# Kernel tuning notes

Measured on AMD Instinct MI355X. Metric: run time of the kernel, lower is better.

Reference implementation:

```python
import jax, jax.numpy as jnp
import numpy as np

N_NODES = 50000
IN_CH = 512
OUT_CH = 512
N_EDGES = 800000


def setup_inputs() -> dict:
    key = jax.random.key(0)
    ks = jax.random.split(key, 6)
    x = jax.random.normal(ks[0], (N_NODES, IN_CH), dtype=jnp.float32)
    edge_index = jax.random.randint(ks[1], (2, N_EDGES), 0, N_NODES, dtype=jnp.int64)
    edge_index_2 = jax.random.randint(ks[2], (2, N_EDGES), 0, N_NODES, dtype=jnp.int64)
    W1 = jax.random.normal(ks[3], (IN_CH, OUT_CH), dtype=jnp.float32) * (1.0 / np.sqrt(IN_CH))
    b1 = jnp.zeros((OUT_CH,), dtype=jnp.float32)
    W2 = jax.random.normal(ks[4], (IN_CH, OUT_CH), dtype=jnp.float32) * (1.0 / np.sqrt(IN_CH))
    b2 = jnp.zeros((OUT_CH,), dtype=jnp.float32)
    return {"x": x, "edge_index": edge_index, "edge_index_2": edge_index_2,
            "W1": W1, "b1": b1, "W2": W2, "b2": b2}


def _sgconv(x, edge_index, W, b, K=2):
    # PyG SGConv: K rounds of D^-1/2 (A+I) D^-1/2 propagation, then Linear.
    N = x.shape[0]
    loops = jnp.arange(N, dtype=edge_index.dtype)
    row = jnp.concatenate([edge_index[0], loops])  # source nodes
    col = jnp.concatenate([edge_index[1], loops])  # destination nodes
    deg = jax.ops.segment_sum(jnp.ones_like(col, dtype=x.dtype), col, num_segments=N)
    deg_inv_sqrt = jnp.where(deg > 0, jnp.where(deg > 0, deg, 1.0) ** -0.5, 0.0)
    norm = deg_inv_sqrt[row] * deg_inv_sqrt[col]  # [E+N]
    h = x
    for _ in range(K):
        h = jax.ops.segment_sum(h[row] * norm[:, None], col, num_segments=N)
    return h @ W + b


def reference(x, edge_index, edge_index_2, W1, b1, W2, b2):
    x1 = _sgconv(x, edge_index, W1, b1)
    x2 = _sgconv(x, edge_index_2, W2, b2)
    logits = jax.nn.softmax(x1, axis=1)
    logits_2 = jax.nn.softmax(x2, axis=1)
    predictions = jnp.argmax(logits, axis=1)
    return (logits, logits_2, predictions)
```

## Files before the change

### kernel.cpp

```cpp
#include <hip/hip_runtime.h>
#include <hip/hip_bf16.h>
#include <cstdint>
#include <cstddef>

#define N_NODES 50000
#define N_EDGES 800000
#define CH 512

typedef __attribute__((ext_vector_type(8))) short bf16x8;
typedef __attribute__((ext_vector_type(4))) float f32x4;

__device__ inline unsigned short f2b(float f) {
    __hip_bfloat16 h = __float2bfloat16(f);
    return *(unsigned short*)&h;
}
__device__ inline float blo(unsigned int u) {
    union { unsigned int i; float f; } v; v.i = u << 16; return v.f;
}
__device__ inline float bhi(unsigned int u) {
    union { unsigned int i; float f; } v; v.i = u & 0xffff0000u; return v.f;
}
__device__ inline unsigned int pack2(unsigned short a, unsigned short b) {
    return (unsigned)a | ((unsigned)b << 16);
}


__global__ __launch_bounds__(256) void count_col(const int* __restrict__ col, int* __restrict__ cnt) {
    int e = blockIdx.x * 256 + threadIdx.x;
    if (e < N_EDGES) atomicAdd(&cnt[col[e]], 1);
}

__global__ __launch_bounds__(256) void make_dinv(const int* __restrict__ cnt, float* __restrict__ dinv) {
    int i = blockIdx.x * 256 + threadIdx.x;
    if (i < N_NODES) dinv[i] = rsqrtf((float)(cnt[i] + 1));
}

__global__ __launch_bounds__(1024) void scan_offsets(const int* __restrict__ cnt, int* __restrict__ offs) {
    __shared__ int wsum[16];
    __shared__ int s_carry;
    int tid = threadIdx.x;
    int lane = tid & 63, wid = tid >> 6;
    if (tid == 0) s_carry = 0;
    __syncthreads();
    const int n = N_NODES;
    for (int c0 = 0; c0 < n; c0 += 1024) {
        int i = c0 + tid;
        int v = (i < n) ? cnt[i] : 0;
        int incl = v;
        #pragma unroll
        for (int d = 1; d < 64; d <<= 1) {
            int t = __shfl_up(incl, d, 64);
            if (lane >= d) incl += t;
        }
        if (lane == 63) wsum[wid] = incl;
        __syncthreads();
        int wbase = 0;
        for (int w = 0; w < wid; ++w) wbase += wsum[w];
        int excl = s_carry + wbase + incl - v;
        if (i < n) offs[i] = excl;
        int ctot = wbase + incl;
        __syncthreads();
        if (tid == 1023) s_carry += ctot;
        __syncthreads();
    }
    if (tid == 0) offs[n] = s_carry;
}

__global__ __launch_bounds__(256) void fill_csr(const int* __restrict__ edges,
                                                const int* __restrict__ offs,
                                                int* __restrict__ cursor,
                                                const float* __restrict__ dinv,
                                                int* __restrict__ srcs,
                                                float* __restrict__ enorm) {
    int e = blockIdx.x * 256 + threadIdx.x;
    if (e >= N_EDGES) return;
    int r = edges[e];
    int c = edges[N_EDGES + e];
    int p = offs[c] + atomicAdd(&cursor[c], 1);
    srcs[p] = r;
    enorm[p] = dinv[r] * dinv[c];
}


__global__ __launch_bounds__(256) void convert_x_bf16(const float* __restrict__ x, unsigned short* __restrict__ xb) {
    int i8 = blockIdx.x * 256 + threadIdx.x;
    const float4* x4 = (const float4*)x;
    float4 a = x4[2 * i8], b = x4[2 * i8 + 1];
    unsigned int o[4];
    o[0] = pack2(f2b(a.x), f2b(a.y));
    o[1] = pack2(f2b(a.z), f2b(a.w));
    o[2] = pack2(f2b(b.x), f2b(b.y));
    o[3] = pack2(f2b(b.z), f2b(b.w));
    ((uint4*)xb)[i8] = make_uint4(o[0], o[1], o[2], o[3]);
}

__global__ __launch_bounds__(256) void convert_w_t(const float* __restrict__ W, unsigned short* __restrict__ Wt) {
    int id = blockIdx.x * 256 + threadIdx.x;
    int k = id >> 9, n = id & 511;
    Wt[(size_t)n * 512 + k] = f2b(W[(size_t)k * 512 + n]);
}

__global__ __launch_bounds__(256) void convert_w_t_split(const float* __restrict__ W,
                                                         unsigned short* __restrict__ Wth,
                                                         unsigned short* __restrict__ Wtl) {
    int id = blockIdx.x * 256 + threadIdx.x;
    int k = id >> 9, n = id & 511;
    float f = W[(size_t)k * 512 + n];
    unsigned short hb = f2b(f);
    union { unsigned int u; float ff; } t; t.u = (unsigned)hb << 16;
    float lo = f - t.ff;
    Wth[(size_t)n * 512 + k] = hb;
    Wtl[(size_t)n * 512 + k] = f2b(lo);
}


__global__ __launch_bounds__(128) void propagate(const float* __restrict__ h, float* __restrict__ out,
                                                 const int* __restrict__ offs,
                                                 const int* __restrict__ srcs,
                                                 const float* __restrict__ enorm,
                                                 const float* __restrict__ dinv) {
    int node = blockIdx.x;
    int t = threadIdx.x;
    const float4* h4 = (const float4*)h;
    float di = dinv[node];
    float w0 = di * di;
    float4 v = h4[(size_t)node * 128 + t];
    float4 acc = make_float4(v.x * w0, v.y * w0, v.z * w0, v.w * w0);
    int e0 = offs[node], e1 = offs[node + 1];
    int e = e0;
    int eu = e0 + ((e1 - e0) & ~3);
    for (; e < eu; e += 4) {
        int s0 = srcs[e], s1 = srcs[e + 1], s2 = srcs[e + 2], s3 = srcs[e + 3];
        float wa = enorm[e], wb = enorm[e + 1], wc = enorm[e + 2], wd = enorm[e + 3];
        float4 u0 = h4[(size_t)s0 * 128 + t];
        float4 u1 = h4[(size_t)s1 * 128 + t];
        float4 u2 = h4[(size_t)s2 * 128 + t];
        float4 u3 = h4[(size_t)s3 * 128 + t];
        acc.x += u0.x * wa; acc.y += u0.y * wa; acc.z += u0.z * wa; acc.w += u0.w * wa;
        acc.x += u1.x * wb; acc.y += u1.y * wb; acc.z += u1.z * wb; acc.w += u1.w * wb;
        acc.x += u2.x * wc; acc.y += u2.y * wc; acc.z += u2.z * wc; acc.w += u2.w * wc;
        acc.x += u3.x * wd; acc.y += u3.y * wd; acc.z += u3.z * wd; acc.w += u3.w * wd;
    }
    for (; e < e1; ++e) {
        int s = srcs[e];
        float w = enorm[e];
        float4 u = h4[(size_t)s * 128 + t];
        acc.x += u.x * w; acc.y += u.y * w; acc.z += u.z * w; acc.w += u.w * w;
    }
    ((float4*)out)[(size_t)node * 128 + t] = acc;
}


__global__ __launch_bounds__(128) void propagate_bf16(const unsigned short* __restrict__ hb,
                                                      unsigned short* __restrict__ outb,
                                                      const int* __restrict__ offs,
                                                      const int* __restrict__ srcs,
                                                      const float* __restrict__ enorm,
                                                      const float* __restrict__ dinv) {
    int node = blockIdx.x * 2 + (threadIdx.x >> 6);
    int lane = threadIdx.x & 63;
    const uint4* h16 = (const uint4*)hb;
    float di = dinv[node];
    float w0 = di * di;
    float acc[8];
    uint4 sv = h16[(size_t)node * 64 + lane];
    acc[0] = blo(sv.x) * w0; acc[1] = bhi(sv.x) * w0;
    acc[2] = blo(sv.y) * w0; acc[3] = bhi(sv.y) * w0;
    acc[4] = blo(sv.z) * w0; acc[5] = bhi(sv.z) * w0;
    acc[6] = blo(sv.w) * w0; acc[7] = bhi(sv.w) * w0;
    int e0 = offs[node], e1 = offs[node + 1];
    int e = e0;
    int eu = e0 + ((e1 - e0) & ~3);
    for (; e < eu; e += 4) {
        int s0 = srcs[e], s1 = srcs[e + 1], s2 = srcs[e + 2], s3 = srcs[e + 3];
        float wa = enorm[e], wb = enorm[e + 1], wc = enorm[e + 2], wd = enorm[e + 3];
        uint4 u0 = h16[(size_t)s0 * 64 + lane];
        uint4 u1 = h16[(size_t)s1 * 64 + lane];
        uint4 u2 = h16[(size_t)s2 * 64 + lane];
        uint4 u3 = h16[(size_t)s3 * 64 + lane];
        acc[0] += blo(u0.x) * wa; acc[1] += bhi(u0.x) * wa;
        acc[2] += blo(u0.y) * wa; acc[3] += bhi(u0.y) * wa;
        acc[4] += blo(u0.z) * wa; acc[5] += bhi(u0.z) * wa;
        acc[6] += blo(u0.w) * wa; acc[7] += bhi(u0.w) * wa;
        acc[0] += blo(u1.x) * wb; acc[1] += bhi(u1.x) * wb;
        acc[2] += blo(u1.y) * wb; acc[3] += bhi(u1.y) * wb;
        acc[4] += blo(u1.z) * wb; acc[5] += bhi(u1.z) * wb;
        acc[6] += blo(u1.w) * wb; acc[7] += bhi(u1.w) * wb;
        acc[0] += blo(u2.x) * wc; acc[1] += bhi(u2.x) * wc;
        acc[2] += blo(u2.y) * wc; acc[3] += bhi(u2.y) * wc;
        acc[4] += blo(u2.z) * wc; acc[5] += bhi(u2.z) * wc;
        acc[6] += blo(u2.w) * wc; acc[7] += bhi(u2.w) * wc;
        acc[0] += blo(u3.x) * wd; acc[1] += bhi(u3.x) * wd;
        acc[2] += blo(u3.y) * wd; acc[3] += bhi(u3.y) * wd;
        acc[4] += blo(u3.z) * wd; acc[5] += bhi(u3.z) * wd;
        acc[6] += blo(u3.w) * wd; acc[7] += bhi(u3.w) * wd;
    }
    for (; e < e1; ++e) {
        int s = srcs[e];
        float w = enorm[e];
        uint4 u = h16[(size_t)s * 64 + lane];
        acc[0] += blo(u.x) * w; acc[1] += bhi(u.x) * w;
        acc[2] += blo(u.y) * w; acc[3] += bhi(u.y) * w;
        acc[4] += blo(u.z) * w; acc[5] += bhi(u.z) * w;
        acc[6] += blo(u.w) * w; acc[7] += bhi(u.w) * w;
    }
    unsigned int o0 = pack2(f2b(acc[0]), f2b(acc[1]));
    unsigned int o1 = pack2(f2b(acc[2]), f2b(acc[3]));
    unsigned int o2 = pack2(f2b(acc[4]), f2b(acc[5]));
    unsigned int o3 = pack2(f2b(acc[6]), f2b(acc[7]));
    ((uint4*)outb)[(size_t)node * 64 + lane] = make_uint4(o0, o1, o2, o3);
}


#define BM2 128
#define BN2 64
#define BK2 32
#define LDP 40

__global__ __launch_bounds__(256) void gemm_bf16(const unsigned short* __restrict__ Ab,
                                                 const unsigned short* __restrict__ Wt,
                                                 const float* __restrict__ bias,
                                                 float* __restrict__ C) {
    __shared__ short Alds[BM2 * LDP];
    __shared__ short Blds[BN2 * LDP];
    int tid = threadIdx.x;
    int lane = tid & 63;
    int wid = tid >> 6;
    int wm = wid & 1;
    int wn = wid >> 1;
    int bm = blockIdx.x * BM2;
    int bn = blockIdx.y * BN2;

    f32x4 acc[4][2] = {};

    int arow0 = tid >> 2, aq = tid & 3;
    int brow = tid >> 2, bq = tid & 3;

    for (int k0 = 0; k0 < CH; k0 += BK2) {
        #pragma unroll
        for (int h = 0; h < 2; ++h) {
            int row = arow0 + h * 64;
            int gr = bm + row;
            uint4 v = make_uint4(0u, 0u, 0u, 0u);
            if (gr < N_NODES) v = *(const uint4*)&Ab[(size_t)gr * CH + k0 + aq * 8];
            *(uint4*)&Alds[row * LDP + aq * 8] = v;
        }
        {
            uint4 v = *(const uint4*)&Wt[(size_t)(bn + brow) * CH + k0 + bq * 8];
            *(uint4*)&Blds[brow * LDP + bq * 8] = v;
        }
        __syncthreads();

        bf16x8 af[4], bf[2];
        #pragma unroll
        for (int mt = 0; mt < 4; ++mt)
            af[mt] = *(const bf16x8*)&Alds[(wm * 64 + mt * 16 + (lane & 15)) * LDP + (lane >> 4) * 8];
        #pragma unroll
        for (int nt = 0; nt < 2; ++nt)
            bf[nt] = *(const bf16x8*)&Blds[(wn * 32 + nt * 16 + (lane & 15)) * LDP + (lane >> 4) * 8];
        #pragma unroll
        for (int mt = 0; mt < 4; ++mt)
            #pragma unroll
            for (int nt = 0; nt < 2; ++nt)
                acc[mt][nt] = __builtin_amdgcn_mfma_f32_16x16x32_bf16(af[mt], bf[nt], acc[mt][nt], 0, 0, 0);
        __syncthreads();
    }

    #pragma unroll
    for (int mt = 0; mt < 4; ++mt) {
        #pragma unroll
        for (int nt = 0; nt < 2; ++nt) {
            int col = bn + wn * 32 + nt * 16 + (lane & 15);
            float bv = bias[col];
            #pragma unroll
            for (int r = 0; r < 4; ++r) {
                int row = bm + wm * 64 + mt * 16 + (lane >> 4) * 4 + r;
                if (row < N_NODES) C[(size_t)row * CH + col] = acc[mt][nt][r] + bv;
            }
        }
    }
}


#define BM3 128
#define BN3 64
#define BK3 32
#define LDP3 40

__global__ __launch_bounds__(256) void gemm_bf16x3(const float* __restrict__ A,
                                                   const unsigned short* __restrict__ Wth,
                                                   const unsigned short* __restrict__ Wtl,
                                                   const float* __restrict__ bias,
                                                   float* __restrict__ C) {
    __shared__ short Ah[BM3 * LDP3];
    __shared__ short Al[BM3 * LDP3];
    __shared__ short Bh[BN3 * LDP3];
    __shared__ short Bl[BN3 * LDP3];
    int tid = threadIdx.x;
    int lane = tid & 63;
    int wid = tid >> 6;
    int wm = wid & 1;
    int wn = wid >> 1;
    int bm = blockIdx.x * BM3;
    int bn = blockIdx.y * BN3;

    f32x4 acc[4][2] = {};

    int arow = tid >> 1, aseg = tid & 1;
    int ga = bm + arow;
    bool aval = ga < N_NODES;
    const float4* A4 = (const float4*)A;
    int brow = tid >> 2, bq = tid & 3;

    for (int k0 = 0; k0 < CH; k0 += BK3) {
        {
            size_t base = (size_t)ga * 128 + (k0 >> 2) + aseg * 4;
            unsigned short h[16], l[16];
            #pragma unroll
            for (int v = 0; v < 4; ++v) {
                float4 f = aval ? A4[base + v] : make_float4(0.f, 0.f, 0.f, 0.f);
                float fs[4] = {f.x, f.y, f.z, f.w};
                #pragma unroll
                for (int j = 0; j < 4; ++j) {
                    unsigned short hb = f2b(fs[j]);
                    union { unsigned int u; float ff; } t; t.u = (unsigned)hb << 16;
                    float lo = fs[j] - t.ff;
                    h[v * 4 + j] = hb;
                    l[v * 4 + j] = f2b(lo);
                }
            }
            uint4 H0 = make_uint4(pack2(h[0], h[1]), pack2(h[2], h[3]), pack2(h[4], h[5]), pack2(h[6], h[7]));
            uint4 H1 = make_uint4(pack2(h[8], h[9]), pack2(h[10], h[11]), pack2(h[12], h[13]), pack2(h[14], h[15]));
            uint4 L0 = make_uint4(pack2(l[0], l[1]), pack2(l[2], l[3]), pack2(l[4], l[5]), pack2(l[6], l[7]));
            uint4 L1 = make_uint4(pack2(l[8], l[9]), pack2(l[10], l[11]), pack2(l[12], l[13]), pack2(l[14], l[15]));
            *(uint4*)&Ah[arow * LDP3 + aseg * 16] = H0;
            *(uint4*)&Ah[arow * LDP3 + aseg * 16 + 8] = H1;
            *(uint4*)&Al[arow * LDP3 + aseg * 16] = L0;
            *(uint4*)&Al[arow * LDP3 + aseg * 16 + 8] = L1;
        }
        *(uint4*)&Bh[brow * LDP3 + bq * 8] = *(const uint4*)&Wth[(size_t)(bn + brow) * CH + k0 + bq * 8];
        *(uint4*)&Bl[brow * LDP3 + bq * 8] = *(const uint4*)&Wtl[(size_t)(bn + brow) * CH + k0 + bq * 8];
        __syncthreads();

        bf16x8 afh[4], afl[4], bfh[2], bfl[2];
        #pragma unroll
        for (int mt = 0; mt < 4; ++mt) {
            int off = (wm * 64 + mt * 16 + (lane & 15)) * LDP3 + (lane >> 4) * 8;
            afh[mt] = *(const bf16x8*)&Ah[off];
            afl[mt] = *(const bf16x8*)&Al[off];
        }
        #pragma unroll
        for (int nt = 0; nt < 2; ++nt) {
            int off = (wn * 32 + nt * 16 + (lane & 15)) * LDP3 + (lane >> 4) * 8;
            bfh[nt] = *(const bf16x8*)&Bh[off];
            bfl[nt] = *(const bf16x8*)&Bl[off];
        }
        #pragma unroll
        for (int mt = 0; mt < 4; ++mt)
            #pragma unroll
            for (int nt = 0; nt < 2; ++nt) {
                acc[mt][nt] = __builtin_amdgcn_mfma_f32_16x16x32_bf16(afh[mt], bfh[nt], acc[mt][nt], 0, 0, 0);
                acc[mt][nt] = __builtin_amdgcn_mfma_f32_16x16x32_bf16(afl[mt], bfh[nt], acc[mt][nt], 0, 0, 0);
                acc[mt][nt] = __builtin_amdgcn_mfma_f32_16x16x32_bf16(afh[mt], bfl[nt], acc[mt][nt], 0, 0, 0);
            }
        __syncthreads();
    }

    #pragma unroll
    for (int mt = 0; mt < 4; ++mt) {
        #pragma unroll
        for (int nt = 0; nt < 2; ++nt) {
            int col = bn + wn * 32 + nt * 16 + (lane & 15);
            float bv = bias[col];
            #pragma unroll
            for (int r = 0; r < 4; ++r) {
                int row = bm + wm * 64 + mt * 16 + (lane >> 4) * 4 + r;
                if (row < N_NODES) C[(size_t)row * CH + col] = acc[mt][nt][r] + bv;
            }
        }
    }
}


#define GAP_THR 2.0e-4f
#define SUSP_CAP 49999

__global__ __launch_bounds__(256) void softmax_rows(const float* __restrict__ X, float* __restrict__ P,
                                                    float* __restrict__ preds,
                                                    int* __restrict__ susp_cnt,
                                                    int* __restrict__ susp_rows) {
    int row = blockIdx.x * 4 + (threadIdx.x >> 6);
    int lane = threadIdx.x & 63;
    if (row >= N_NODES) return;
    const float4* x4 = (const float4*)(X + (size_t)row * CH);
    float4 v0 = x4[lane];
    float4 v1 = x4[lane + 64];
    float vals[8] = {v0.x, v0.y, v0.z, v0.w, v1.x, v1.y, v1.z, v1.w};
    float m = vals[0];
    float m2 = -INFINITY;
    int mi = lane * 4;
    #pragma unroll
    for (int j = 1; j < 8; ++j) {
        int c = (j < 4) ? (lane * 4 + j) : (256 + lane * 4 + (j - 4));
        if (vals[j] > m) { m2 = m; m = vals[j]; mi = c; }
        else if (vals[j] > m2) { m2 = vals[j]; }
    }
    #pragma unroll
    for (int d = 32; d > 0; d >>= 1) {
        float om = __shfl_xor(m, d, 64);
        int oi = __shfl_xor(mi, d, 64);
        float om2 = __shfl_xor(m2, d, 64);
        if (om > m || (om == m && oi < mi)) {
            m2 = fmaxf(m, om2);
            m = om; mi = oi;
        } else {
            m2 = fmaxf(m2, om);
        }
    }
    float s = 0.f;
    float ex[8];
    #pragma unroll
    for (int j = 0; j < 8; ++j) { ex[j] = __expf(vals[j] - m); s += ex[j]; }
    #pragma unroll
    for (int d = 32; d > 0; d >>= 1) s += __shfl_xor(s, d, 64);
    float inv = 1.0f / s;
    float4 o0 = make_float4(ex[0] * inv, ex[1] * inv, ex[2] * inv, ex[3] * inv);
    float4 o1 = make_float4(ex[4] * inv, ex[5] * inv, ex[6] * inv, ex[7] * inv);
    float4* p4 = (float4*)(P + (size_t)row * CH);
    p4[lane] = o0;
    p4[lane + 64] = o1;
    if (preds != nullptr && lane == 0) {
        preds[row] = (float)mi;
        if (m - m2 < GAP_THR) {
            int p = atomicAdd(susp_cnt, 1);
            if (p < SUSP_CAP) susp_rows[p] = row;
        }
    }
}


__global__ __launch_bounds__(256) void fix_preds(const float* __restrict__ A, const float* __restrict__ W,
                                                 const float* __restrict__ bias,
                                                 const int* __restrict__ susp_cnt,
                                                 const int* __restrict__ susp_rows,
                                                 float* __restrict__ preds) {
    __shared__ float rowbuf[8][512];
    __shared__ float rbest[8][4];
    __shared__ int ridx[8][4];
    int cnt = *susp_cnt;
    if (cnt > SUSP_CAP) cnt = SUSP_CAP;
    int tid = threadIdx.x, lane = tid & 63, wid = tid >> 6;
    for (int base = blockIdx.x * 8; base < cnt; base += gridDim.x * 8) {
        int nr = min(8, cnt - base);
        __syncthreads();
        for (int r = 0; r < nr; ++r) {
            int row = susp_rows[base + r];
            if (tid < 128) ((float4*)rowbuf[r])[tid] = ((const float4*)&A[(size_t)row * 512])[tid];
        }
        __syncthreads();
        float best[8]; int bidx[8];
        #pragma unroll
        for (int r = 0; r < 8; ++r) { best[r] = -INFINITY; bidx[r] = 0; }
        for (int cc = 0; cc < 2; ++cc) {
            int c = cc * 256 + tid;
            float bv = bias[c];
            float s[8];
            #pragma unroll
            for (int r = 0; r < 8; ++r) s[r] = bv;
            #pragma unroll 8
            for (int k = 0; k < 512; ++k) {
                float w = W[(size_t)k * 512 + c];
                #pragma unroll
                for (int r = 0; r < 8; ++r) s[r] += rowbuf[r][k] * w;
            }
            #pragma unroll
            for (int r = 0; r < 8; ++r)
                if (s[r] > best[r]) { best[r] = s[r]; bidx[r] = c; }
        }
        #pragma unroll
        for (int r = 0; r < 8; ++r) {
            float b = best[r]; int i = bidx[r];
            #pragma unroll
            for (int d = 32; d > 0; d >>= 1) {
                float ob = __shfl_xor(b, d, 64);
                int oi = __shfl_xor(i, d, 64);
                if (ob > b || (ob == b && oi < i)) { b = ob; i = oi; }
            }
            if (lane == 0) { rbest[r][wid] = b; ridx[r][wid] = i; }
        }
        __syncthreads();
        if (tid < nr) {
            int r = tid;
            float b = rbest[r][0]; int i = ridx[r][0];
            #pragma unroll
            for (int w = 1; w < 4; ++w) {
                if (rbest[r][w] > b || (rbest[r][w] == b && ridx[r][w] < i)) { b = rbest[r][w]; i = ridx[r][w]; }
            }
            preds[susp_rows[base + r]] = (float)i;
        }
    }
}


extern "C" void kernel_launch(void* const* d_in, const int* in_sizes, int n_in,
                              void* d_out, int out_size, void* d_ws, size_t ws_size,
                              hipStream_t stream) {
    const float* x  = (const float*)d_in[0];
    const int*   e1 = (const int*)d_in[1];
    const int*   e2 = (const int*)d_in[2];
    const float* W1 = (const float*)d_in[3];
    const float* b1 = (const float*)d_in[4];
    const float* W2 = (const float*)d_in[5];
    const float* b2 = (const float*)d_in[6];

    float* out     = (float*)d_out;
    float* logits1 = out;
    float* logits2 = out + (size_t)N_NODES * CH;
    float* preds   = out + 2 * (size_t)N_NODES * CH;

    const size_t NEED = 109600016;
    if (ws_size < NEED) return;

    char* ws = (char*)d_ws;
    float* A      = (float*)(ws);
    int*   cnt    = (int*)(ws + 102400000);
    int*   offs   = (int*)(ws + 102600000);
    int*   cursor = (int*)(ws + 102800016);
    float* dinv   = (float*)(ws + 103000016);
    int*   srcs   = (int*)(ws + 103200016);
    float* enorm  = (float*)(ws + 106400016);

    unsigned short* xb  = (unsigned short*)logits1;
    unsigned short* Wtb = (unsigned short*)((char*)logits1 + 51200000);
    unsigned short* h1b = (unsigned short*)A;
    unsigned short* h2b = (unsigned short*)((char*)A + 51200000);

    unsigned short* Wt1h = (unsigned short*)srcs;
    unsigned short* Wt1l = (unsigned short*)enorm;
    int* susp_cnt  = (int*)cursor;
    int* susp_rows = (int*)cursor + 1;

    {
        hipMemsetAsync(cnt, 0, N_NODES * sizeof(int), stream);
        hipMemsetAsync(cursor, 0, N_NODES * sizeof(int), stream);
        count_col<<<(N_EDGES + 255) / 256, 256, 0, stream>>>(e2 + N_EDGES, cnt);
        make_dinv<<<(N_NODES + 255) / 256, 256, 0, stream>>>(cnt, dinv);
        scan_offsets<<<1, 1024, 0, stream>>>(cnt, offs);
        fill_csr<<<(N_EDGES + 255) / 256, 256, 0, stream>>>(e2, offs, cursor, dinv, srcs, enorm);

        convert_x_bf16<<<(N_NODES * CH / 8 + 255) / 256, 256, 0, stream>>>(x, xb);
        convert_w_t<<<(512 * 512) / 256, 256, 0, stream>>>(W2, Wtb);

        propagate_bf16<<<N_NODES / 2, 128, 0, stream>>>(xb, h1b, offs, srcs, enorm, dinv);
        propagate_bf16<<<N_NODES / 2, 128, 0, stream>>>(h1b, h2b, offs, srcs, enorm, dinv);

        dim3 g((N_NODES + BM2 - 1) / BM2, CH / BN2);
        gemm_bf16<<<g, 256, 0, stream>>>(h2b, Wtb, b2, logits2);
        softmax_rows<<<N_NODES / 4, 256, 0, stream>>>(logits2, logits2, nullptr, nullptr, nullptr);
    }

    {
        hipMemsetAsync(cnt, 0, N_NODES * sizeof(int), stream);
        hipMemsetAsync(cursor, 0, N_NODES * sizeof(int), stream);
        count_col<<<(N_EDGES + 255) / 256, 256, 0, stream>>>(e1 + N_EDGES, cnt);
        make_dinv<<<(N_NODES + 255) / 256, 256, 0, stream>>>(cnt, dinv);
        scan_offsets<<<1, 1024, 0, stream>>>(cnt, offs);
        fill_csr<<<(N_EDGES + 255) / 256, 256, 0, stream>>>(e1, offs, cursor, dinv, srcs, enorm);

        propagate<<<N_NODES, 128, 0, stream>>>(x, logits1, offs, srcs, enorm, dinv);
        propagate<<<N_NODES, 128, 0, stream>>>(logits1, A, offs, srcs, enorm, dinv);

        convert_w_t_split<<<(512 * 512) / 256, 256, 0, stream>>>(W1, Wt1h, Wt1l);
        hipMemsetAsync(susp_cnt, 0, sizeof(int), stream);

        dim3 g((N_NODES + BM3 - 1) / BM3, CH / BN3);
        gemm_bf16x3<<<g, 256, 0, stream>>>(A, Wt1h, Wt1l, b1, logits1);
        softmax_rows<<<N_NODES / 4, 256, 0, stream>>>(logits1, logits1, preds, susp_cnt, susp_rows);
        fix_preds<<<400, 256, 0, stream>>>(A, W1, b1, susp_cnt, susp_rows, preds);
    }
}
```

Before: 1.749 ms.

## Widen GEMM tiles to 256 columns, unroll gathers by 8, fold dinv into scan

```diff
diff --git a/kernel.cpp b/kernel.cpp
--- a/kernel.cpp
+++ b/kernel.cpp
@@ -30,12 +30,8 @@
     if (e < N_EDGES) atomicAdd(&cnt[col[e]], 1);
 }
 
-__global__ __launch_bounds__(256) void make_dinv(const int* __restrict__ cnt, float* __restrict__ dinv) {
-    int i = blockIdx.x * 256 + threadIdx.x;
-    if (i < N_NODES) dinv[i] = rsqrtf((float)(cnt[i] + 1));
-}
-
-__global__ __launch_bounds__(1024) void scan_offsets(const int* __restrict__ cnt, int* __restrict__ offs) {
+__global__ __launch_bounds__(1024) void scan_offsets(const int* __restrict__ cnt, int* __restrict__ offs,
+                                                     float* __restrict__ dinv) {
     __shared__ int wsum[16];
     __shared__ int s_carry;
     int tid = threadIdx.x;
@@ -46,6 +42,7 @@
     for (int c0 = 0; c0 < n; c0 += 1024) {
         int i = c0 + tid;
         int v = (i < n) ? cnt[i] : 0;
+        if (i < n) dinv[i] = rsqrtf((float)(v + 1));
         int incl = v;
         #pragma unroll
         for (int d = 1; d < 64; d <<= 1) {
@@ -128,18 +125,19 @@
     float4 acc = make_float4(v.x * w0, v.y * w0, v.z * w0, v.w * w0);
     int e0 = offs[node], e1 = offs[node + 1];
     int e = e0;
-    int eu = e0 + ((e1 - e0) & ~3);
-    for (; e < eu; e += 4) {
-        int s0 = srcs[e], s1 = srcs[e + 1], s2 = srcs[e + 2], s3 = srcs[e + 3];
-        float wa = enorm[e], wb = enorm[e + 1], wc = enorm[e + 2], wd = enorm[e + 3];
-        float4 u0 = h4[(size_t)s0 * 128 + t];
-        float4 u1 = h4[(size_t)s1 * 128 + t];
-        float4 u2 = h4[(size_t)s2 * 128 + t];
-        float4 u3 = h4[(size_t)s3 * 128 + t];
-        acc.x += u0.x * wa; acc.y += u0.y * wa; acc.z += u0.z * wa; acc.w += u0.w * wa;
-        acc.x += u1.x * wb; acc.y += u1.y * wb; acc.z += u1.z * wb; acc.w += u1.w * wb;
-        acc.x += u2.x * wc; acc.y += u2.y * wc; acc.z += u2.z * wc; acc.w += u2.w * wc;
-        acc.x += u3.x * wd; acc.y += u3.y * wd; acc.z += u3.z * wd; acc.w += u3.w * wd;
+    int eu = e0 + ((e1 - e0) & ~7);
+    for (; e < eu; e += 8) {
+        int s[8]; float w[8];
+        #pragma unroll
+        for (int q = 0; q < 8; ++q) { s[q] = srcs[e + q]; w[q] = enorm[e + q]; }
+        float4 u[8];
+        #pragma unroll
+        for (int q = 0; q < 8; ++q) u[q] = h4[(size_t)s[q] * 128 + t];
+        #pragma unroll
+        for (int q = 0; q < 8; ++q) {
+            acc.x += u[q].x * w[q]; acc.y += u[q].y * w[q];
+            acc.z += u[q].z * w[q]; acc.w += u[q].w * w[q];
+        }
     }
     for (; e < e1; ++e) {
         int s = srcs[e];
@@ -170,30 +168,21 @@
     acc[6] = blo(sv.w) * w0; acc[7] = bhi(sv.w) * w0;
     int e0 = offs[node], e1 = offs[node + 1];
     int e = e0;
-    int eu = e0 + ((e1 - e0) & ~3);
-    for (; e < eu; e += 4) {
-        int s0 = srcs[e], s1 = srcs[e + 1], s2 = srcs[e + 2], s3 = srcs[e + 3];
-        float wa = enorm[e], wb = enorm[e + 1], wc = enorm[e + 2], wd = enorm[e + 3];
-        uint4 u0 = h16[(size_t)s0 * 64 + lane];
-        uint4 u1 = h16[(size_t)s1 * 64 + lane];
-        uint4 u2 = h16[(size_t)s2 * 64 + lane];
-        uint4 u3 = h16[(size_t)s3 * 64 + lane];
-        acc[0] += blo(u0.x) * wa; acc[1] += bhi(u0.x) * wa;
-        acc[2] += blo(u0.y) * wa; acc[3] += bhi(u0.y) * wa;
-        acc[4] += blo(u0.z) * wa; acc[5] += bhi(u0.z) * wa;
-        acc[6] += blo(u0.w) * wa; acc[7] += bhi(u0.w) * wa;
-        acc[0] += blo(u1.x) * wb; acc[1] += bhi(u1.x) * wb;
-        acc[2] += blo(u1.y) * wb; acc[3] += bhi(u1.y) * wb;
-        acc[4] += blo(u1.z) * wb; acc[5] += bhi(u1.z) * wb;
-        acc[6] += blo(u1.w) * wb; acc[7] += bhi(u1.w) * wb;
-        acc[0] += blo(u2.x) * wc; acc[1] += bhi(u2.x) * wc;
-        acc[2] += blo(u2.y) * wc; acc[3] += bhi(u2.y) * wc;
-        acc[4] += blo(u2.z) * wc; acc[5] += bhi(u2.z) * wc;
-        acc[6] += blo(u2.w) * wc; acc[7] += bhi(u2.w) * wc;
-        acc[0] += blo(u3.x) * wd; acc[1] += bhi(u3.x) * wd;
-        acc[2] += blo(u3.y) * wd; acc[3] += bhi(u3.y) * wd;
-        acc[4] += blo(u3.z) * wd; acc[5] += bhi(u3.z) * wd;
-        acc[6] += blo(u3.w) * wd; acc[7] += bhi(u3.w) * wd;
+    int eu = e0 + ((e1 - e0) & ~7);
+    for (; e < eu; e += 8) {
+        int s[8]; float w[8];
+        #pragma unroll
+        for (int q = 0; q < 8; ++q) { s[q] = srcs[e + q]; w[q] = enorm[e + q]; }
+        uint4 u[8];
+        #pragma unroll
+        for (int q = 0; q < 8; ++q) u[q] = h16[(size_t)s[q] * 64 + lane];
+        #pragma unroll
+        for (int q = 0; q < 8; ++q) {
+            acc[0] += blo(u[q].x) * w[q]; acc[1] += bhi(u[q].x) * w[q];
+            acc[2] += blo(u[q].y) * w[q]; acc[3] += bhi(u[q].y) * w[q];
+            acc[4] += blo(u[q].z) * w[q]; acc[5] += bhi(u[q].z) * w[q];
+            acc[6] += blo(u[q].w) * w[q]; acc[7] += bhi(u[q].w) * w[q];
+        }
     }
     for (; e < e1; ++e) {
         int s = srcs[e];
@@ -213,11 +202,11 @@
 
 
 #define BM2 128
-#define BN2 64
+#define BN2 256
 #define BK2 32
 #define LDP 40
 
-__global__ __launch_bounds__(256) void gemm_bf16(const unsigned short* __restrict__ Ab,
+__global__ __launch_bounds__(512) void gemm_bf16(const unsigned short* __restrict__ Ab,
                                                  const unsigned short* __restrict__ Wt,
                                                  const float* __restrict__ bias,
                                                  float* __restrict__ C) {
@@ -231,37 +220,37 @@
     int bm = blockIdx.x * BM2;
     int bn = blockIdx.y * BN2;
 
-    f32x4 acc[4][2] = {};
-
-    int arow0 = tid >> 2, aq = tid & 3;
-    int brow = tid >> 2, bq = tid & 3;
+    f32x4 acc[4][4] = {};
+
+    int arow = tid >> 2, ak8 = (tid & 3) * 8;
+    int brow = tid >> 1, bk16 = (tid & 1) * 16;
+    int ga = bm + arow;
+    bool aval = ga < N_NODES;
 
     for (int k0 = 0; k0 < CH; k0 += BK2) {
-        #pragma unroll
-        for (int h = 0; h < 2; ++h) {
-            int row = arow0 + h * 64;
-            int gr = bm + row;
+        {
             uint4 v = make_uint4(0u, 0u, 0u, 0u);
-            if (gr < N_NODES) v = *(const uint4*)&Ab[(size_t)gr * CH + k0 + aq * 8];
-            *(uint4*)&Alds[row * LDP + aq * 8] = v;
+            if (aval) v = *(const uint4*)&Ab[(size_t)ga * CH + k0 + ak8];
+            *(uint4*)&Alds[arow * LDP + ak8] = v;
         }
         {
-            uint4 v = *(const uint4*)&Wt[(size_t)(bn + brow) * CH + k0 + bq * 8];
-            *(uint4*)&Blds[brow * LDP + bq * 8] = v;
-        }
-        __syncthreads();
-
-        bf16x8 af[4], bf[2];
+            const unsigned short* s = &Wt[(size_t)(bn + brow) * CH + k0 + bk16];
+            *(uint4*)&Blds[brow * LDP + bk16] = *(const uint4*)s;
+            *(uint4*)&Blds[brow * LDP + bk16 + 8] = *(const uint4*)(s + 8);
+        }
+        __syncthreads();
+
+        bf16x8 af[4], bf[4];
         #pragma unroll
         for (int mt = 0; mt < 4; ++mt)
             af[mt] = *(const bf16x8*)&Alds[(wm * 64 + mt * 16 + (lane & 15)) * LDP + (lane >> 4) * 8];
         #pragma unroll
-        for (int nt = 0; nt < 2; ++nt)
-            bf[nt] = *(const bf16x8*)&Blds[(wn * 32 + nt * 16 + (lane & 15)) * LDP + (lane >> 4) * 8];
+        for (int nt = 0; nt < 4; ++nt)
+            bf[nt] = *(const bf16x8*)&Blds[(wn * 64 + nt * 16 + (lane & 15)) * LDP + (lane >> 4) * 8];
         #pragma unroll
         for (int mt = 0; mt < 4; ++mt)
             #pragma unroll
-            for (int nt = 0; nt < 2; ++nt)
+            for (int nt = 0; nt < 4; ++nt)
                 acc[mt][nt] = __builtin_amdgcn_mfma_f32_16x16x32_bf16(af[mt], bf[nt], acc[mt][nt], 0, 0, 0);
         __syncthreads();
     }
@@ -269,8 +258,8 @@
     #pragma unroll
     for (int mt = 0; mt < 4; ++mt) {
         #pragma unroll
-        for (int nt = 0; nt < 2; ++nt) {
-            int col = bn + wn * 32 + nt * 16 + (lane & 15);
+        for (int nt = 0; nt < 4; ++nt) {
+            int col = bn + wn * 64 + nt * 16 + (lane & 15);
             float bv = bias[col];
             #pragma unroll
             for (int r = 0; r < 4; ++r) {
@@ -283,11 +272,11 @@
 
 
 #define BM3 128
-#define BN3 64
+#define BN3 256
 #define BK3 32
 #define LDP3 40
 
-__global__ __launch_bounds__(256) void gemm_bf16x3(const float* __restrict__ A,
+__global__ __launch_bounds__(512) void gemm_bf16x3(const float* __restrict__ A,
                                                    const unsigned short* __restrict__ Wth,
                                                    const unsigned short* __restrict__ Wtl,
                                                    const float* __restrict__ bias,
@@ -304,45 +293,44 @@
     int bm = blockIdx.x * BM3;
     int bn = blockIdx.y * BN3;
 
-    f32x4 acc[4][2] = {};
-
-    int arow = tid >> 1, aseg = tid & 1;
+    f32x4 acc[4][4] = {};
+
+    int arow = tid >> 2, ak8 = (tid & 3) * 8;
+    int brow = tid >> 1, bk16 = (tid & 1) * 16;
     int ga = bm + arow;
     bool aval = ga < N_NODES;
-    const float4* A4 = (const float4*)A;
-    int brow = tid >> 2, bq = tid & 3;
 
     for (int k0 = 0; k0 < CH; k0 += BK3) {
         {
-            size_t base = (size_t)ga * 128 + (k0 >> 2) + aseg * 4;
-            unsigned short h[16], l[16];
-            #pragma unroll
-            for (int v = 0; v < 4; ++v) {
-                float4 f = aval ? A4[base + v] : make_float4(0.f, 0.f, 0.f, 0.f);
-                float fs[4] = {f.x, f.y, f.z, f.w};
-                #pragma unroll
-                for (int j = 0; j < 4; ++j) {
-                    unsigned short hb = f2b(fs[j]);
-                    union { unsigned int u; float ff; } t; t.u = (unsigned)hb << 16;
-                    float lo = fs[j] - t.ff;
-                    h[v * 4 + j] = hb;
-                    l[v * 4 + j] = f2b(lo);
-                }
-            }
-            uint4 H0 = make_uint4(pack2(h[0], h[1]), pack2(h[2], h[3]), pack2(h[4], h[5]), pack2(h[6], h[7]));
-            uint4 H1 = make_uint4(pack2(h[8], h[9]), pack2(h[10], h[11]), pack2(h[12], h[13]), pack2(h[14], h[15]));
-            uint4 L0 = make_uint4(pack2(l[0], l[1]), pack2(l[2], l[3]), pack2(l[4], l[5]), pack2(l[6], l[7]));
-            uint4 L1 = make_uint4(pack2(l[8], l[9]), pack2(l[10], l[11]), pack2(l[12], l[13]), pack2(l[14], l[15]));
-            *(uint4*)&Ah[arow * LDP3 + aseg * 16] = H0;
-            *(uint4*)&Ah[arow * LDP3 + aseg * 16 + 8] = H1;
-            *(uint4*)&Al[arow * LDP3 + aseg * 16] = L0;
-            *(uint4*)&Al[arow * LDP3 + aseg * 16 + 8] = L1;
-        }
-        *(uint4*)&Bh[brow * LDP3 + bq * 8] = *(const uint4*)&Wth[(size_t)(bn + brow) * CH + k0 + bq * 8];
-        *(uint4*)&Bl[brow * LDP3 + bq * 8] = *(const uint4*)&Wtl[(size_t)(bn + brow) * CH + k0 + bq * 8];
-        __syncthreads();
-
-        bf16x8 afh[4], afl[4], bfh[2], bfl[2];
+            const float* src = &A[(size_t)ga * CH + k0 + ak8];
+            float4 f0 = aval ? *(const float4*)(src)     : make_float4(0.f, 0.f, 0.f, 0.f);
+            float4 f1 = aval ? *(const float4*)(src + 4) : make_float4(0.f, 0.f, 0.f, 0.f);
+            float fs[8] = {f0.x, f0.y, f0.z, f0.w, f1.x, f1.y, f1.z, f1.w};
+            unsigned short h[8], l[8];
+            #pragma unroll
+            for (int j = 0; j < 8; ++j) {
+                unsigned short hb = f2b(fs[j]);
+                union { unsigned int u; float ff; } t; t.u = (unsigned)hb << 16;
+                float lo = fs[j] - t.ff;
+                h[j] = hb;
+                l[j] = f2b(lo);
+            }
+            *(uint4*)&Ah[arow * LDP3 + ak8] =
+                make_uint4(pack2(h[0], h[1]), pack2(h[2], h[3]), pack2(h[4], h[5]), pack2(h[6], h[7]));
+            *(uint4*)&Al[arow * LDP3 + ak8] =
+                make_uint4(pack2(l[0], l[1]), pack2(l[2], l[3]), pack2(l[4], l[5]), pack2(l[6], l[7]));
+        }
+        {
+            const unsigned short* sh = &Wth[(size_t)(bn + brow) * CH + k0 + bk16];
+            const unsigned short* sl = &Wtl[(size_t)(bn + brow) * CH + k0 + bk16];
+            *(uint4*)&Bh[brow * LDP3 + bk16]     = *(const uint4*)sh;
+            *(uint4*)&Bh[brow * LDP3 + bk16 + 8] = *(const uint4*)(sh + 8);
+            *(uint4*)&Bl[brow * LDP3 + bk16]     = *(const uint4*)sl;
+            *(uint4*)&Bl[brow * LDP3 + bk16 + 8] = *(const uint4*)(sl + 8);
+        }
+        __syncthreads();
+
+        bf16x8 afh[4], afl[4], bfh[4], bfl[4];
         #pragma unroll
         for (int mt = 0; mt < 4; ++mt) {
             int off = (wm * 64 + mt * 16 + (lane & 15)) * LDP3 + (lane >> 4) * 8;
@@ -350,15 +338,15 @@
             afl[mt] = *(const bf16x8*)&Al[off];
         }
         #pragma unroll
-        for (int nt = 0; nt < 2; ++nt) {
-            int off = (wn * 32 + nt * 16 + (lane & 15)) * LDP3 + (lane >> 4) * 8;
+        for (int nt = 0; nt < 4; ++nt) {
+            int off = (wn * 64 + nt * 16 + (lane & 15)) * LDP3 + (lane >> 4) * 8;
             bfh[nt] = *(const bf16x8*)&Bh[off];
             bfl[nt] = *(const bf16x8*)&Bl[off];
         }
         #pragma unroll
         for (int mt = 0; mt < 4; ++mt)
             #pragma unroll
-            for (int nt = 0; nt < 2; ++nt) {
+            for (int nt = 0; nt < 4; ++nt) {
                 acc[mt][nt] = __builtin_amdgcn_mfma_f32_16x16x32_bf16(afh[mt], bfh[nt], acc[mt][nt], 0, 0, 0);
                 acc[mt][nt] = __builtin_amdgcn_mfma_f32_16x16x32_bf16(afl[mt], bfh[nt], acc[mt][nt], 0, 0, 0);
                 acc[mt][nt] = __builtin_amdgcn_mfma_f32_16x16x32_bf16(afh[mt], bfl[nt], acc[mt][nt], 0, 0, 0);
@@ -369,8 +357,8 @@
     #pragma unroll
     for (int mt = 0; mt < 4; ++mt) {
         #pragma unroll
-        for (int nt = 0; nt < 2; ++nt) {
-            int col = bn + wn * 32 + nt * 16 + (lane & 15);
+        for (int nt = 0; nt < 4; ++nt) {
+            int col = bn + wn * 64 + nt * 16 + (lane & 15);
             float bv = bias[col];
             #pragma unroll
             for (int r = 0; r < 4; ++r) {
@@ -544,8 +532,7 @@
         hipMemsetAsync(cnt, 0, N_NODES * sizeof(int), stream);
         hipMemsetAsync(cursor, 0, N_NODES * sizeof(int), stream);
         count_col<<<(N_EDGES + 255) / 256, 256, 0, stream>>>(e2 + N_EDGES, cnt);
-        make_dinv<<<(N_NODES + 255) / 256, 256, 0, stream>>>(cnt, dinv);
-        scan_offsets<<<1, 1024, 0, stream>>>(cnt, offs);
+        scan_offsets<<<1, 1024, 0, stream>>>(cnt, offs, dinv);
         fill_csr<<<(N_EDGES + 255) / 256, 256, 0, stream>>>(e2, offs, cursor, dinv, srcs, enorm);
 
         convert_x_bf16<<<(N_NODES * CH / 8 + 255) / 256, 256, 0, stream>>>(x, xb);
@@ -555,7 +542,7 @@
         propagate_bf16<<<N_NODES / 2, 128, 0, stream>>>(h1b, h2b, offs, srcs, enorm, dinv);
 
         dim3 g((N_NODES + BM2 - 1) / BM2, CH / BN2);
-        gemm_bf16<<<g, 256, 0, stream>>>(h2b, Wtb, b2, logits2);
+        gemm_bf16<<<g, 512, 0, stream>>>(h2b, Wtb, b2, logits2);
         softmax_rows<<<N_NODES / 4, 256, 0, stream>>>(logits2, logits2, nullptr, nullptr, nullptr);
     }
 
@@ -563,8 +550,7 @@
         hipMemsetAsync(cnt, 0, N_NODES * sizeof(int), stream);
         hipMemsetAsync(cursor, 0, N_NODES * sizeof(int), stream);
         count_col<<<(N_EDGES + 255) / 256, 256, 0, stream>>>(e1 + N_EDGES, cnt);
-        make_dinv<<<(N_NODES + 255) / 256, 256, 0, stream>>>(cnt, dinv);
-        scan_offsets<<<1, 1024, 0, stream>>>(cnt, offs);
+        scan_offsets<<<1, 1024, 0, stream>>>(cnt, offs, dinv);
         fill_csr<<<(N_EDGES + 255) / 256, 256, 0, stream>>>(e1, offs, cursor, dinv, srcs, enorm);
 
         propagate<<<N_NODES, 128, 0, stream>>>(x, logits1, offs, srcs, enorm, dinv);
@@ -574,7 +560,7 @@
         hipMemsetAsync(susp_cnt, 0, sizeof(int), stream);
 
         dim3 g((N_NODES + BM3 - 1) / BM3, CH / BN3);
-        gemm_bf16x3<<<g, 256, 0, stream>>>(A, Wt1h, Wt1l, b1, logits1);
+        gemm_bf16x3<<<g, 512, 0, stream>>>(A, Wt1h, Wt1l, b1, logits1);
         softmax_rows<<<N_NODES / 4, 256, 0, stream>>>(logits1, logits1, preds, susp_cnt, susp_rows);
         fix_preds<<<400, 256, 0, stream>>>(A, W1, b1, susp_cnt, susp_rows, preds);
     }
```

Result: faster. 1.676 ms (-4.2%).
